# Kernel optimization log

Hardware: AMD Instinct MI355X
Metric: run time of the kernel (lower is better)

Reference implementation:

```python
import jax, jax.numpy as jnp
import numpy as np

N = 100000       # num nodes
E = 1600000      # num edges (before self loops)
IN = 128         # in_channels
H = 4            # heads (layer 1)
C = 64           # hidden_channels
BN_EPS = 1e-5
NEG_SLOPE = 0.2  # PyG GATConv default


def setup_inputs() -> dict:
    key = jax.random.key(0)
    ks = jax.random.split(key, 12)
    s = lambda k, shape: jax.random.normal(k, shape, jnp.float32) * 0.05
    return {
        "x": jax.random.normal(ks[0], (N, IN), jnp.float32),
        "edge_index": jax.random.randint(ks[1], (2, E), 0, N),
        # GATConv layer 1: in=128 -> 64 per head, 4 heads, concat
        "W1": s(ks[2], (IN, H * C)),
        "a_src1": s(ks[3], (H, C)),
        "a_dst1": s(ks[4], (H, C)),
        "b1": jnp.zeros((H * C,), jnp.float32),
        # BatchNorm1d(256), eval mode with default running stats
        "bn_gamma": jnp.ones((H * C,), jnp.float32),
        "bn_beta": jnp.zeros((H * C,), jnp.float32),
        # GATConv layer 2: 256 -> 1, heads=1, concat=False
        "W2": s(ks[5], (H * C, 1)),
        "a_src2": s(ks[6], (1, 1)),
        "a_dst2": s(ks[7], (1, 1)),
        "b2": jnp.zeros((1,), jnp.float32),
        # risk predictor MLP: Linear(1,64) -> ReLU -> Linear(64,1) -> Sigmoid
        "mlp_w1": s(ks[8], (1, C)),
        "mlp_b1": jnp.zeros((C,), jnp.float32),
        "mlp_w2": s(ks[9], (C, 1)),
        "mlp_b2": jnp.zeros((1,), jnp.float32),
    }


def gat_conv(x, W, a_s, a_d, b, src, dst, n, concat):
    """PyG-style GATConv (self loops already appended to src/dst)."""
    h_, c_ = a_s.shape
    h = (x @ W).reshape(n, h_, c_)                       # [N,H,C]
    alpha_src = jnp.einsum('nhc,hc->nh', h, a_s)          # [N,H]
    alpha_dst = jnp.einsum('nhc,hc->nh', h, a_d)          # [N,H]
    alpha = jax.nn.leaky_relu(alpha_src[src] + alpha_dst[dst], NEG_SLOPE)  # [E,H]
    # segment softmax over destination nodes (self loops guarantee nonempty segments)
    amax = jax.ops.segment_max(alpha, dst, num_segments=n)
    ex = jnp.exp(alpha - amax[dst])
    den = jax.ops.segment_sum(ex, dst, num_segments=n)
    coef = ex / den[dst]                                  # [E,H]
    out = jax.ops.segment_sum(h[src] * coef[..., None], dst, num_segments=n)  # [N,H,C]
    out = out.reshape(n, h_ * c_) if concat else out.mean(axis=1)
    return out + b


def reference(x, edge_index, W1, a_src1, a_dst1, b1, bn_gamma, bn_beta,
              W2, a_src2, a_dst2, b2, mlp_w1, mlp_b1, mlp_w2, mlp_b2):
    n = x.shape[0]
    loops = jnp.arange(n)
    src = jnp.concatenate([edge_index[0], loops])
    dst = jnp.concatenate([edge_index[1], loops])

    h = gat_conv(x, W1, a_src1, a_dst1, b1, src, dst, n, concat=True)   # [N,256]
    # BatchNorm1d eval: running_mean=0, running_var=1
    h = h / jnp.sqrt(jnp.float32(1.0 + BN_EPS)) * bn_gamma + bn_beta
    h = jax.nn.elu(h)
    # dropout is identity in eval mode
    h = gat_conv(h, W2, a_src2, a_dst2, b2, src, dst, n, concat=False)  # [N,1]

    risk = jax.nn.relu(h @ mlp_w1 + mlp_b1)
    risk = jax.nn.sigmoid(risk @ mlp_w2 + mlp_b2)                        # [N,1]
    return risk
```

## Files before the change

kernel.cpp:

```cpp
#include <hip/hip_runtime.h>
#include <math.h>

#define NSL 0.2f
#define BSH 8
#define CAP 4608
#define ECHUNK 4096
#define MAXNB 512

typedef __attribute__((ext_vector_type(8))) short bf16x8;
typedef __attribute__((ext_vector_type(4))) float f32x4;
typedef __attribute__((ext_vector_type(2))) float floatx2;

__device__ __forceinline__ unsigned short f2b(float f){
  unsigned int u = __builtin_bit_cast(unsigned int, f);
  u = (u + 0x7FFFu + ((u >> 16) & 1u)) >> 16;
  return (unsigned short)u;
}
__device__ __forceinline__ unsigned cvtpk_bf16(float a, float b){
  unsigned r; asm("v_cvt_pk_bf16_f32 %0, %1, %2" : "=v"(r) : "v"(a), "v"(b)); return r;
}
__device__ __forceinline__ void pkfma(floatx2& a, floatx2 x, floatx2 w){
  asm("v_pk_fma_f32 %0, %1, %2, %0" : "+v"(a) : "v"(x), "v"(w));
}

__global__ void k_binit(int* gCur, int NB){
  int i = blockIdx.x*blockDim.x + threadIdx.x;
  if (i < NB) gCur[i] = i*CAP;
}

__global__ __launch_bounds__(256) void k_bucket(const int* __restrict__ esrc, const int* __restrict__ edst,
                                                int E, int NB, int* gCur, unsigned* __restrict__ ebuf){
  __shared__ int hist[MAXNB];
  __shared__ int base[MAXNB];
  int t = threadIdx.x;
  for (int i=t;i<NB;i+=256) hist[i] = 0;
  __syncthreads();
  int e0 = blockIdx.x*ECHUNK;
  int srcv[16], dstv[16];
  #pragma unroll
  for (int j=0;j<16;j++){
    int e = e0 + t + j*256;
    if (e < E){ srcv[j] = esrc[e]; dstv[j] = edst[e]; atomicAdd(&hist[dstv[j]>>BSH], 1); }
    else dstv[j] = -1;
  }
  __syncthreads();
  for (int i=t;i<NB;i+=256){
    int h = hist[i];
    base[i] = h > 0 ? atomicAdd(&gCur[i], h) : 0;
    hist[i] = 0;
  }
  __syncthreads();
  #pragma unroll
  for (int j=0;j<16;j++){
    if (dstv[j] >= 0){
      int b = dstv[j]>>BSH;
      int pos = base[b] + atomicAdd(&hist[b], 1);
      if (pos < (b+1)*CAP)
        ebuf[pos] = (unsigned)srcv[j] | ((unsigned)(dstv[j] & 255) << 17);
    }
  }
}

__global__ __launch_bounds__(256) void k_csr(const int* __restrict__ gCur, const unsigned* __restrict__ ebuf,
                                             const float* __restrict__ as4, const float* __restrict__ ad4,
                                             int* __restrict__ rows, int* __restrict__ deg,
                                             int* __restrict__ csr, float* __restrict__ wgt4, int N){
  __shared__ int lcnt[256];
  __shared__ int rofs[256];
  __shared__ int csr_l[CAP+256];
  __shared__ unsigned char dl_l[CAP+256];
  int b = blockIdx.x, t = threadIdx.x;
  int node0 = b<<BSH;
  int nNodes = min(256, N - node0);
  int cnt_b = min(gCur[b] - b*CAP, CAP);
  lcnt[t] = 0;
  __syncthreads();
  const unsigned* eb = ebuf + (size_t)b*CAP;
  for (int i=t;i<cnt_b;i+=256) atomicAdd(&lcnt[eb[i]>>17], 1);
  __syncthreads();
  int v = (t < nNodes) ? (lcnt[t] + 1) : 0;
  rofs[t] = v; __syncthreads();
  #pragma unroll
  for (int o=1;o<256;o<<=1){
    int x = (t>=o) ? rofs[t-o] : 0; __syncthreads();
    rofs[t] += x; __syncthreads();
  }
  int excl = rofs[t] - v;
  if (t < nNodes){ csr_l[excl] = node0 + t; dl_l[excl] = (unsigned char)t; }
  lcnt[t] = excl + 1;
  __syncthreads();
  for (int i=t;i<cnt_b;i+=256){
    unsigned e = eb[i];
    int dl = e >> 17;
    int pos = atomicAdd(&lcnt[dl], 1);
    csr_l[pos] = (int)(e & 0x1FFFFu);
    dl_l[pos]  = (unsigned char)dl;
  }
  __syncthreads();
  int total = rofs[255];
  int gbase = b*(CAP+256);
  for (int i=t;i<total;i+=256){
    int src = csr_l[i];
    int dl  = dl_l[i];
    float4 av = *(const float4*)&as4[(size_t)src*4];
    float4 dv = *(const float4*)&ad4[(size_t)(node0+dl)*4];
    float ax = av.x+dv.x, ay = av.y+dv.y, az = av.z+dv.z, aw = av.w+dv.w;
    ax = fmaxf(ax, NSL*ax); ay = fmaxf(ay, NSL*ay);
    az = fmaxf(az, NSL*az); aw = fmaxf(aw, NSL*aw);
    float4 w4 = { __expf(ax), __expf(ay), __expf(az), __expf(aw) };
    *(float4*)&wgt4[(size_t)(gbase+i)*4] = w4;
    csr[gbase+i] = src;
  }
  if (t < nNodes){ rows[node0+t] = gbase + excl; deg[node0+t] = v; }
}

__global__ __launch_bounds__(256) void k_prep_w(const float* __restrict__ W, unsigned short* __restrict__ wt){
  int idx = blockIdx.x*256 + threadIdx.x;
  int k = idx >> 8, ch = idx & 255;
  wt[ch*128 + k] = f2b(W[idx]);
}

__global__ __launch_bounds__(256) void k_gemm1(const unsigned short* __restrict__ w1t,
                                               const float* __restrict__ x,
                                               const float* __restrict__ a_s1,
                                               const float* __restrict__ a_d1,
                                               unsigned char* __restrict__ h1f8,
                                               float* __restrict__ asrc, float* __restrict__ adst,
                                               int N){
  __shared__ unsigned short xs[64][132];
  int tid = threadIdx.x;
  int lane = tid & 63, w = tid >> 6;
  int g = lane >> 4, nr = lane & 15;
  int n0 = blockIdx.x*64;

  #pragma unroll
  for (int i=0;i<8;i++){
    int idx = tid + i*256;
    int node = idx >> 5, c4 = idx & 31;
    int gn = n0 + node;
    float4 v = (gn < N) ? *(const float4*)&x[(size_t)gn*128 + c4*4] : make_float4(0,0,0,0);
    uint2 pk = { cvtpk_bf16(v.x, v.y), cvtpk_bf16(v.z, v.w) };
    *(uint2*)&xs[node][c4*4] = pk;
  }
  __syncthreads();

  int node_f[4]; bool val_f[4];
  #pragma unroll
  for (int fn=0;fn<4;fn++){ node_f[fn] = n0 + fn*16 + nr; val_f[fn] = node_f[fn] < N; }

  f32x4 acc[4][4] = {};
  #pragma unroll
  for (int s=0;s<4;s++){
    int ks = s*32;
    bf16x8 af[4], bf[4];
    #pragma unroll
    for (int fm=0;fm<4;fm++){
      int ch = w*64 + fm*16 + nr;
      const ushort4 lo = *(const ushort4*)(w1t + ch*128 + ks + 4*g);
      const ushort4 hi = *(const ushort4*)(w1t + ch*128 + ks + 16 + 4*g);
      af[fm] = (bf16x8){ (short)lo.x,(short)lo.y,(short)lo.z,(short)lo.w,
                         (short)hi.x,(short)hi.y,(short)hi.z,(short)hi.w };
    }
    #pragma unroll
    for (int fn=0;fn<4;fn++){
      union { uint2 u2[2]; bf16x8 v; } bb;
      bb.u2[0] = *(const uint2*)&xs[fn*16 + nr][ks + 4*g];
      bb.u2[1] = *(const uint2*)&xs[fn*16 + nr][ks + 16 + 4*g];
      bf[fn] = bb.v;
    }
    #pragma unroll
    for (int fm=0;fm<4;fm++)
      #pragma unroll
      for (int fn=0;fn<4;fn++)
        acc[fm][fn] = __builtin_amdgcn_mfma_f32_16x16x32_bf16(af[fm], bf[fn], acc[fm][fn], 0, 0, 0);
  }

  float ps[4] = {0.f,0.f,0.f,0.f}, pd[4] = {0.f,0.f,0.f,0.f};
  #pragma unroll
  for (int fm=0;fm<4;fm++){
    int cb = w*64 + fm*16 + g*4;
    float4 av = *(const float4*)&a_s1[cb];
    float4 dv = *(const float4*)&a_d1[cb];
    #pragma unroll
    for (int fn=0;fn<4;fn++){
      f32x4 c = acc[fm][fn];
      if (val_f[fn]){
        int u = __builtin_amdgcn_cvt_pk_fp8_f32(c[0], c[1], 0, false);
        u = __builtin_amdgcn_cvt_pk_fp8_f32(c[2], c[3], u, true);
        *(unsigned int*)(h1f8 + (size_t)node_f[fn]*256 + cb) = (unsigned int)u;
      }
      ps[fn] += c[0]*av.x + c[1]*av.y + c[2]*av.z + c[3]*av.w;
      pd[fn] += c[0]*dv.x + c[1]*dv.y + c[2]*dv.z + c[3]*dv.w;
    }
  }
  #pragma unroll
  for (int fn=0;fn<4;fn++){
    ps[fn] += __shfl_xor(ps[fn], 16); ps[fn] += __shfl_xor(ps[fn], 32);
    pd[fn] += __shfl_xor(pd[fn], 16); pd[fn] += __shfl_xor(pd[fn], 32);
    if (g == 0 && val_f[fn]){
      asrc[node_f[fn]*4 + w] = ps[fn];
      adst[node_f[fn]*4 + w] = pd[fn];
    }
  }
}

__global__ __launch_bounds__(256) void k_agg1(const int* __restrict__ rows, const int* __restrict__ deg,
                                              const int* __restrict__ csr,
                                              const float* __restrict__ wgtf,
                                              const unsigned char* __restrict__ h1f8,
                                              const float* __restrict__ b1,
                                              const float* __restrict__ gamma, const float* __restrict__ beta,
                                              const float* __restrict__ W2,
                                              float* __restrict__ h2, int N){
  int lane = threadIdx.x & 63, wv = threadIdx.x >> 6;
  int node = blockIdx.x*4 + wv;
  if (node >= N) return;
  int slot = lane >> 4, l4 = lane & 15;
  int head = l4 >> 2;
  int rs = rows[node], d = deg[node];
  const uint4* h1u4 = (const uint4*)h1f8;
  floatx2 acc2[8];
  #pragma unroll
  for (int j=0;j<8;j++){ acc2[j][0] = 0.f; acc2[j][1] = 0.f; }
  float den = 0.f;
  int nit = (d + 3) >> 2;

  auto ldS = [&](int k)->int  { int i = slot + 4*k; return (i < d) ? csr[rs+i] : 0; };
  auto ldW = [&](int k)->float{ int i = slot + 4*k; return (i < d) ? wgtf[(size_t)(rs+i)*4 + head] : 0.f; };

  int   sA = ldS(0), sB = ldS(1);
  int   s2 = ldS(2), s3 = ldS(3);
  float w0 = ldW(0), w1 = ldW(1), w2 = ldW(2), w3 = ldW(3);
  uint4 v0 = h1u4[(size_t)sA*16 + l4];
  uint4 v1 = h1u4[(size_t)sB*16 + l4];

  for (int it=0; it<nit; ++it){
    int   sn = ldS(it+4);
    float wn = ldW(it+4);
    uint4 vn = h1u4[(size_t)s2*16 + l4];
    den += w0;
    floatx2 ww; ww[0] = w0; ww[1] = w0;
    floatx2 f;
    f = __builtin_amdgcn_cvt_pk_f32_fp8(v0.x, false); pkfma(acc2[0], f, ww);
    f = __builtin_amdgcn_cvt_pk_f32_fp8(v0.x, true ); pkfma(acc2[1], f, ww);
    f = __builtin_amdgcn_cvt_pk_f32_fp8(v0.y, false); pkfma(acc2[2], f, ww);
    f = __builtin_amdgcn_cvt_pk_f32_fp8(v0.y, true ); pkfma(acc2[3], f, ww);
    f = __builtin_amdgcn_cvt_pk_f32_fp8(v0.z, false); pkfma(acc2[4], f, ww);
    f = __builtin_amdgcn_cvt_pk_f32_fp8(v0.z, true ); pkfma(acc2[5], f, ww);
    f = __builtin_amdgcn_cvt_pk_f32_fp8(v0.w, false); pkfma(acc2[6], f, ww);
    f = __builtin_amdgcn_cvt_pk_f32_fp8(v0.w, true ); pkfma(acc2[7], f, ww);
    v0 = v1; v1 = vn;
    s2 = s3; s3 = sn;
    w0 = w1; w1 = w2; w2 = w3; w3 = wn;
  }

  #pragma unroll
  for (int j=0;j<8;j++){
    acc2[j][0] += __shfl_xor(acc2[j][0],16); acc2[j][1] += __shfl_xor(acc2[j][1],16);
    acc2[j][0] += __shfl_xor(acc2[j][0],32); acc2[j][1] += __shfl_xor(acc2[j][1],32);
  }
  den += __shfl_xor(den,16); den += __shfl_xor(den,32);
  float inv = 1.f/den;
  const float bsc = 0.99999500003749968f;
  int c = l4*16;
  float p = 0.f;
  #pragma unroll
  for (int q=0;q<4;q++){
    int cq = c + q*4;
    float4 bb = *(const float4*)&b1[cq];
    float4 gg = *(const float4*)&gamma[cq];
    float4 be = *(const float4*)&beta[cq];
    float4 w2_ = *(const float4*)&W2[cq];
    float o0 = (acc2[q*2+0][0]*inv + bb.x)*bsc*gg.x + be.x;
    float o1 = (acc2[q*2+0][1]*inv + bb.y)*bsc*gg.y + be.y;
    float o2 = (acc2[q*2+1][0]*inv + bb.z)*bsc*gg.z + be.z;
    float o3 = (acc2[q*2+1][1]*inv + bb.w)*bsc*gg.w + be.w;
    o0 = (o0>0.f)?o0:(__expf(o0)-1.f); o1 = (o1>0.f)?o1:(__expf(o1)-1.f);
    o2 = (o2>0.f)?o2:(__expf(o2)-1.f); o3 = (o3>0.f)?o3:(__expf(o3)-1.f);
    p += o0*w2_.x + o1*w2_.y + o2*w2_.z + o3*w2_.w;
  }
  p += __shfl_xor(p,1); p += __shfl_xor(p,2); p += __shfl_xor(p,4); p += __shfl_xor(p,8);
  if (lane == 0) h2[node] = p;
}

__global__ __launch_bounds__(256) void k_agg2(const int* __restrict__ rows, const int* __restrict__ deg,
                       const int* __restrict__ csr, const float* __restrict__ h2,
                       const float* __restrict__ as2, const float* __restrict__ ad2,
                       const float* __restrict__ b2,
                       const float* __restrict__ mw1, const float* __restrict__ mb1,
                       const float* __restrict__ mw2, const float* __restrict__ mb2,
                       float* __restrict__ out, int N){
  int t = threadIdx.x;
  int g16 = t >> 4, l = t & 15;
  int n = blockIdx.x*16 + g16;
  if (n >= N) return;
  float a_s = as2[0], a_d = ad2[0];
  float hd = h2[n];
  float ad = hd * a_d;
  int rs = rows[n], d = deg[n];
  float den = 0.f, num = 0.f;
  for (int i=l;i<d;i+=16){
    int s = csr[rs+i];
    float hs = h2[s];
    float al = hs*a_s + ad;
    al = fmaxf(al, NSL*al);
    float w = __expf(al);
    den += w; num += w*hs;
  }
  #pragma unroll
  for (int o=1;o<16;o<<=1){ den += __shfl_xor(den,o); num += __shfl_xor(num,o); }
  float o2 = num/den + b2[0];
  float acc = 0.f;
  #pragma unroll
  for (int q=0;q<4;q++){
    int j = l + q*16;
    float r = fmaxf(o2*mw1[j] + mb1[j], 0.f);
    acc += r*mw2[j];
  }
  #pragma unroll
  for (int o=1;o<16;o<<=1) acc += __shfl_xor(acc,o);
  if (l == 0) out[n] = 1.f/(1.f + __expf(-(acc + mb2[0])));
}

extern "C" void kernel_launch(void* const* d_in, const int* in_sizes, int n_in,
                              void* d_out, int out_size, void* d_ws, size_t ws_size,
                              hipStream_t stream){
  const float* x   = (const float*)d_in[0];
  const int*   ei  = (const int*)  d_in[1];
  const float* W1  = (const float*)d_in[2];
  const float* as1 = (const float*)d_in[3];
  const float* ad1 = (const float*)d_in[4];
  const float* b1  = (const float*)d_in[5];
  const float* gam = (const float*)d_in[6];
  const float* bet = (const float*)d_in[7];
  const float* W2  = (const float*)d_in[8];
  const float* as2 = (const float*)d_in[9];
  const float* ad2 = (const float*)d_in[10];
  const float* b2  = (const float*)d_in[11];
  const float* mw1 = (const float*)d_in[12];
  const float* mb1 = (const float*)d_in[13];
  const float* mw2 = (const float*)d_in[14];
  const float* mb2 = (const float*)d_in[15];
  float* out = (float*)d_out;

  int N = in_sizes[0] / 128;
  int E = in_sizes[1] / 2;
  const int* esrc = ei;
  const int* edst = ei + E;
  int NB = (N + 255) >> 8;

  char* p = (char*)d_ws;
  auto alloc = [&](size_t bytes)->char*{ char* r = p; p += (bytes + 255) & ~(size_t)255; return r; };
  int*      deg   = (int*)     alloc((size_t)N*4);
  int*      rows  = (int*)     alloc((size_t)N*4);
  int*      gCur  = (int*)     alloc((size_t)NB*4);
  unsigned* ebuf  = (unsigned*)alloc((size_t)NB*CAP*4);
  int*      csr   = (int*)     alloc((size_t)NB*(CAP+256)*4);
  float*    wgt4  = (float*)   alloc((size_t)NB*(CAP+256)*16);
  unsigned short* w1t  = (unsigned short*)alloc((size_t)256*128*2);
  unsigned char*  h1f8 = (unsigned char*) alloc((size_t)N*256);
  float* asrc  = (float*)alloc((size_t)N*4*4);
  float* adst  = (float*)alloc((size_t)N*4*4);
  float* h2    = (float*)alloc((size_t)N*4);

  k_binit<<<(NB+255)/256,256,0,stream>>>(gCur, NB);
  int nbA = (E + ECHUNK - 1)/ECHUNK;
  k_bucket<<<nbA,256,0,stream>>>(esrc, edst, E, NB, gCur, ebuf);

  k_prep_w<<<128,256,0,stream>>>(W1, w1t);
  k_gemm1<<<(N+63)/64,256,0,stream>>>(w1t, x, as1, ad1, h1f8, asrc, adst, N);

  k_csr<<<NB,256,0,stream>>>(gCur, ebuf, asrc, adst, rows, deg, csr, wgt4, N);

  k_agg1<<<(N+3)/4,256,0,stream>>>(rows, deg, csr, wgt4, h1f8, b1, gam, bet, W2, h2, N);

  k_agg2<<<(N+15)/16,256,0,stream>>>(rows, deg, csr, h2, as2, ad2, b2, mw1, mb1, mw2, mb2, out, N);
}
```

Baseline: 236.1 us.

## Pack edge source and bf16 attention weights into one record for aggregation

Replaces the separate csr index and fp32 per-head weight arrays read by the first aggregation kernel with a single 16-byte record per edge holding the source id and four bf16 exp-weights. The agg loop is restructured to load one record per edge, with a two-stage software pipeline and masking by degree instead of per-load bounds checks. Pad records after each bucket are zeroed so over-reads stay valid. It also merges the bucket-cursor init into the weight-prep kernel to drop one launch. Storing the weights in bf16 lowers their precision.

```diff
diff --git a/kernel.cpp b/kernel.cpp
--- a/kernel.cpp
+++ b/kernel.cpp
@@ -23,9 +23,12 @@
   asm("v_pk_fma_f32 %0, %1, %2, %0" : "+v"(a) : "v"(x), "v"(w));
 }
 
-__global__ void k_binit(int* gCur, int NB){
-  int i = blockIdx.x*blockDim.x + threadIdx.x;
-  if (i < NB) gCur[i] = i*CAP;
+__global__ __launch_bounds__(256) void k_prep(const float* __restrict__ W, unsigned short* __restrict__ wt,
+                                              int* gCur, int NB){
+  int idx = blockIdx.x*256 + threadIdx.x;
+  int k = idx >> 8, ch = idx & 255;
+  wt[ch*128 + k] = f2b(W[idx]);
+  if (idx < NB) gCur[idx] = idx*CAP;
 }
 
 __global__ __launch_bounds__(256) void k_bucket(const int* __restrict__ esrc, const int* __restrict__ edst,
@@ -64,7 +67,7 @@
 __global__ __launch_bounds__(256) void k_csr(const int* __restrict__ gCur, const unsigned* __restrict__ ebuf,
                                              const float* __restrict__ as4, const float* __restrict__ ad4,
                                              int* __restrict__ rows, int* __restrict__ deg,
-                                             int* __restrict__ csr, float* __restrict__ wgt4, int N){
+                                             int* __restrict__ csr, uint4* __restrict__ rec, int N){
   __shared__ int lcnt[256];
   __shared__ int rofs[256];
   __shared__ int csr_l[CAP+256];
@@ -107,17 +110,19 @@
     float ax = av.x+dv.x, ay = av.y+dv.y, az = av.z+dv.z, aw = av.w+dv.w;
     ax = fmaxf(ax, NSL*ax); ay = fmaxf(ay, NSL*ay);
     az = fmaxf(az, NSL*az); aw = fmaxf(aw, NSL*aw);
-    float4 w4 = { __expf(ax), __expf(ay), __expf(az), __expf(aw) };
-    *(float4*)&wgt4[(size_t)(gbase+i)*4] = w4;
+    uint4 r;
+    r.x = (unsigned)src;
+    r.y = cvtpk_bf16(__expf(ax), __expf(ay));
+    r.z = cvtpk_bf16(__expf(az), __expf(aw));
+    r.w = 0u;
+    rec[gbase+i] = r;
     csr[gbase+i] = src;
   }
+  if (t < 16){
+    int p = total + t;
+    if (p < CAP+256) rec[gbase+p] = (uint4){0u,0u,0u,0u};
+  }
   if (t < nNodes){ rows[node0+t] = gbase + excl; deg[node0+t] = v; }
-}
-
-__global__ __launch_bounds__(256) void k_prep_w(const float* __restrict__ W, unsigned short* __restrict__ wt){
-  int idx = blockIdx.x*256 + threadIdx.x;
-  int k = idx >> 8, ch = idx & 255;
-  wt[ch*128 + k] = f2b(W[idx]);
 }
 
 __global__ __launch_bounds__(256) void k_gemm1(const unsigned short* __restrict__ w1t,
@@ -205,8 +210,7 @@
 }
 
 __global__ __launch_bounds__(256) void k_agg1(const int* __restrict__ rows, const int* __restrict__ deg,
-                                              const int* __restrict__ csr,
-                                              const float* __restrict__ wgtf,
+                                              const uint4* __restrict__ rec,
                                               const unsigned char* __restrict__ h1f8,
                                               const float* __restrict__ b1,
                                               const float* __restrict__ gamma, const float* __restrict__ beta,
@@ -217,42 +221,53 @@
   if (node >= N) return;
   int slot = lane >> 4, l4 = lane & 15;
   int head = l4 >> 2;
+  bool h23 = head >= 2;
+  bool hhi = (head & 1) != 0;
   int rs = rows[node], d = deg[node];
+  int dms = d - slot;
+  const uint4* recp = rec + rs;
   const uint4* h1u4 = (const uint4*)h1f8;
   floatx2 acc2[8];
   #pragma unroll
   for (int j=0;j<8;j++){ acc2[j][0] = 0.f; acc2[j][1] = 0.f; }
   float den = 0.f;
-  int nit = (d + 3) >> 2;
-
-  auto ldS = [&](int k)->int  { int i = slot + 4*k; return (i < d) ? csr[rs+i] : 0; };
-  auto ldW = [&](int k)->float{ int i = slot + 4*k; return (i < d) ? wgtf[(size_t)(rs+i)*4 + head] : 0.f; };
-
-  int   sA = ldS(0), sB = ldS(1);
-  int   s2 = ldS(2), s3 = ldS(3);
-  float w0 = ldW(0), w1 = ldW(1), w2 = ldW(2), w3 = ldW(3);
-  uint4 v0 = h1u4[(size_t)sA*16 + l4];
-  uint4 v1 = h1u4[(size_t)sB*16 + l4];
-
-  for (int it=0; it<nit; ++it){
-    int   sn = ldS(it+4);
-    float wn = ldW(it+4);
-    uint4 vn = h1u4[(size_t)s2*16 + l4];
-    den += w0;
-    floatx2 ww; ww[0] = w0; ww[1] = w0;
+  int nj = (d + 3) >> 2;
+
+  auto step = [&](const uint4& r, const uint4& v, int t4){
+    unsigned ws = h23 ? r.z : r.y;
+    unsigned hw = hhi ? (ws & 0xFFFF0000u) : (ws << 16);
+    float w = __builtin_bit_cast(float, hw);
+    w = (t4 < dms) ? w : 0.f;
+    den += w;
+    floatx2 ww; ww[0] = w; ww[1] = w;
     floatx2 f;
-    f = __builtin_amdgcn_cvt_pk_f32_fp8(v0.x, false); pkfma(acc2[0], f, ww);
-    f = __builtin_amdgcn_cvt_pk_f32_fp8(v0.x, true ); pkfma(acc2[1], f, ww);
-    f = __builtin_amdgcn_cvt_pk_f32_fp8(v0.y, false); pkfma(acc2[2], f, ww);
-    f = __builtin_amdgcn_cvt_pk_f32_fp8(v0.y, true ); pkfma(acc2[3], f, ww);
-    f = __builtin_amdgcn_cvt_pk_f32_fp8(v0.z, false); pkfma(acc2[4], f, ww);
-    f = __builtin_amdgcn_cvt_pk_f32_fp8(v0.z, true ); pkfma(acc2[5], f, ww);
-    f = __builtin_amdgcn_cvt_pk_f32_fp8(v0.w, false); pkfma(acc2[6], f, ww);
-    f = __builtin_amdgcn_cvt_pk_f32_fp8(v0.w, true ); pkfma(acc2[7], f, ww);
-    v0 = v1; v1 = vn;
-    s2 = s3; s3 = sn;
-    w0 = w1; w1 = w2; w2 = w3; w3 = wn;
-  }
+    f = __builtin_amdgcn_cvt_pk_f32_fp8(v.x, false); pkfma(acc2[0], f, ww);
+    f = __builtin_amdgcn_cvt_pk_f32_fp8(v.x, true ); pkfma(acc2[1], f, ww);
+    f = __builtin_amdgcn_cvt_pk_f32_fp8(v.y, false); pkfma(acc2[2], f, ww);
+    f = __builtin_amdgcn_cvt_pk_f32_fp8(v.y, true ); pkfma(acc2[3], f, ww);
+    f = __builtin_amdgcn_cvt_pk_f32_fp8(v.z, false); pkfma(acc2[4], f, ww);
+    f = __builtin_amdgcn_cvt_pk_f32_fp8(v.z, true ); pkfma(acc2[5], f, ww);
+    f = __builtin_amdgcn_cvt_pk_f32_fp8(v.w, false); pkfma(acc2[6], f, ww);
+    f = __builtin_amdgcn_cvt_pk_f32_fp8(v.w, true ); pkfma(acc2[7], f, ww);
+  };
+
+  uint4 rA = recp[slot];
+  uint4 rB = recp[slot + 4];
+  uint4 vA = h1u4[(size_t)rA.x*16 + l4];
+  uint4 vB = h1u4[(size_t)rB.x*16 + l4];
+
+  int t = 0;
+  for (; t + 2 <= nj; t += 2){
+    uint4 rA2 = recp[slot + 4*t + 8];
+    step(rA, vA, 4*t);
+    vA = h1u4[(size_t)rA2.x*16 + l4];
+    rA = rA2;
+    uint4 rB2 = recp[slot + 4*t + 12];
+    step(rB, vB, 4*t + 4);
+    vB = h1u4[(size_t)rB2.x*16 + l4];
+    rB = rB2;
+  }
+  if (t < nj) step(rA, vA, 4*t);
 
   #pragma unroll
   for (int j=0;j<8;j++){
@@ -356,23 +371,22 @@
   int*      gCur  = (int*)     alloc((size_t)NB*4);
   unsigned* ebuf  = (unsigned*)alloc((size_t)NB*CAP*4);
   int*      csr   = (int*)     alloc((size_t)NB*(CAP+256)*4);
-  float*    wgt4  = (float*)   alloc((size_t)NB*(CAP+256)*16);
+  uint4*    rec   = (uint4*)   alloc((size_t)NB*(CAP+256)*16 + 256);
   unsigned short* w1t  = (unsigned short*)alloc((size_t)256*128*2);
   unsigned char*  h1f8 = (unsigned char*) alloc((size_t)N*256);
   float* asrc  = (float*)alloc((size_t)N*4*4);
   float* adst  = (float*)alloc((size_t)N*4*4);
   float* h2    = (float*)alloc((size_t)N*4);
 
-  k_binit<<<(NB+255)/256,256,0,stream>>>(gCur, NB);
+  k_prep<<<128,256,0,stream>>>(W1, w1t, gCur, NB);
   int nbA = (E + ECHUNK - 1)/ECHUNK;
   k_bucket<<<nbA,256,0,stream>>>(esrc, edst, E, NB, gCur, ebuf);
 
-  k_prep_w<<<128,256,0,stream>>>(W1, w1t);
   k_gemm1<<<(N+63)/64,256,0,stream>>>(w1t, x, as1, ad1, h1f8, asrc, adst, N);
 
-  k_csr<<<NB,256,0,stream>>>(gCur, ebuf, asrc, adst, rows, deg, csr, wgt4, N);
-
-  k_agg1<<<(N+3)/4,256,0,stream>>>(rows, deg, csr, wgt4, h1f8, b1, gam, bet, W2, h2, N);
+  k_csr<<<NB,256,0,stream>>>(gCur, ebuf, asrc, adst, rows, deg, csr, rec, N);
+
+  k_agg1<<<(N+3)/4,256,0,stream>>>(rows, deg, rec, h1f8, b1, gam, bet, W2, h2, N);
 
   k_agg2<<<(N+15)/16,256,0,stream>>>(rows, deg, csr, h2, as2, ad2, b2, mw1, mb1, mw2, mb2, out, N);
 }
```

Measured after the change: 237.8 us. About the same (+0.7%).
